# Kernel tuning notes

Measured on AMD Instinct MI355X. Metric: run time of the kernel, lower is better.

The kernel has to match this reference:

```python
import jax, jax.numpy as jnp
import numpy as np
from jax import lax

IMG = 512            # image H = W
FH = FW = 32         # feature map spatial size
A = 9                # anchors per location (3 sizes x 3 ratios)
N = FH * FW * A      # total anchors = 9216
IOU_THR = 0.7
MIN_SCORE = 0.5
MIN_SIZE = 1e-3


def make_anchors():
    """Anchors in centroid format (cx, cy, w, h), ordered (H, W, A)."""
    stride = IMG / FH
    sizes = np.array([32.0, 64.0, 128.0])
    ratios = np.array([0.5, 1.0, 2.0])
    ws = (sizes[:, None] / np.sqrt(ratios)[None, :]).reshape(-1)  # (A,)
    hs = (sizes[:, None] * np.sqrt(ratios)[None, :]).reshape(-1)  # (A,)
    cx = (np.arange(FW) + 0.5) * stride
    cy = (np.arange(FH) + 0.5) * stride
    CX = np.broadcast_to(cx[None, :, None], (FH, FW, A))
    CY = np.broadcast_to(cy[:, None, None], (FH, FW, A))
    Wg = np.broadcast_to(ws[None, None, :], (FH, FW, A))
    Hg = np.broadcast_to(hs[None, None, :], (FH, FW, A))
    anc = np.stack([CX, CY, Wg, Hg], axis=-1).reshape(-1, 4)
    return jnp.asarray(anc, dtype=jnp.float32)


def pairwise_iou(b):
    # b: (N,4) corners x1,y1,x2,y2
    x1, y1, x2, y2 = b[:, 0], b[:, 1], b[:, 2], b[:, 3]
    area = (x2 - x1) * (y2 - y1)
    ix1 = jnp.maximum(x1[:, None], x1[None, :])
    iy1 = jnp.maximum(y1[:, None], y1[None, :])
    ix2 = jnp.minimum(x2[:, None], x2[None, :])
    iy2 = jnp.minimum(y2[:, None], y2[None, :])
    inter = jnp.maximum(ix2 - ix1, 0.0) * jnp.maximum(iy2 - iy1, 0.0)
    union = area[:, None] + area[None, :] - inter
    return inter / jnp.maximum(union, 1e-9)


def nms_keep(boxes, scores, valid):
    """Greedy NMS. Returns bool keep mask of shape (N,). Index decisions only."""
    s = jnp.where(valid, scores, -jnp.inf)
    order = jnp.argsort(-s)
    b = boxes[order]
    v = valid[order]
    ious = pairwise_iou(b)  # (N, N)
    idx = jnp.arange(N)

    def body(i, supp):
        keep_i = (~supp[i]) & v[i]
        return supp | (keep_i & (ious[i] > IOU_THR) & (idx > i))

    supp = lax.fori_loop(0, N, body, jnp.zeros(N, dtype=bool))
    keep_sorted = (~supp) & v
    return jnp.zeros(N, dtype=bool).at[order].set(keep_sorted)


def setup_inputs() -> dict:
    key = jax.random.key(0)
    ks = jax.random.split(key, 4)
    return {
        "feature_map": jax.random.normal(ks[0], (1, 256, FH, FW), jnp.float32),
        "conv1_w": jax.random.normal(ks[1], (512, 256, 3, 3), jnp.float32) * 0.02,
        "conv1_b": jnp.zeros((512,), jnp.float32),
        "conv2_w": jax.random.normal(ks[2], (A, 512), jnp.float32) * 0.01,
        "conv2_b": jnp.zeros((A,), jnp.float32),
        "conv3_w": jax.random.normal(ks[3], (4 * A, 512), jnp.float32) * 0.01,
        "conv3_b": jnp.zeros((4 * A,), jnp.float32),
    }


def reference(feature_map, conv1_w, conv1_b, conv2_w, conv2_b, conv3_w, conv3_b):
    anchors = make_anchors()  # (N,4) cx,cy,w,h

    # --- conv backbone head ---
    h = lax.conv_general_dilated(
        feature_map, conv1_w, (1, 1), "SAME",
        dimension_numbers=("NCHW", "OIHW", "NCHW"))
    h = jax.nn.relu(h + conv1_b[None, :, None, None])  # (1,512,H,W)

    scores = jax.nn.sigmoid(
        jnp.einsum("bchw,ac->bahw", h, conv2_w) + conv2_b[None, :, None, None])
    scores = scores.transpose(0, 2, 3, 1).reshape(-1)  # (N,) ordered (H,W,A)

    off = jnp.einsum("bchw,oc->bohw", h, conv3_w) + conv3_b[None, :, None, None]
    off = off.reshape(1, A, 4, FH, FW).transpose(0, 3, 4, 1, 2).reshape(-1, 4)

    acx, acy, aw, ah = anchors[:, 0], anchors[:, 1], anchors[:, 2], anchors[:, 3]
    cx = acx + off[:, 0] * aw
    cy = acy + off[:, 1] * ah
    bw = aw * jnp.exp(off[:, 2])
    bh = ah * jnp.exp(off[:, 3])
    boxes = jnp.stack([cx - bw / 2, cy - bh / 2, cx + bw / 2, cy + bh / 2], axis=1)

    # --- clip to image ---
    lo = jnp.array([0.0, 0.0, 0.0, 0.0], jnp.float32)
    hi = jnp.array([IMG, IMG, IMG, IMG], jnp.float32)
    boxes = jnp.clip(boxes, lo, hi)

    # --- remove small boxes + score threshold (as a mask, jit-safe) ---
    valid = ((boxes[:, 2] - boxes[:, 0]) >= MIN_SIZE) \
          & ((boxes[:, 3] - boxes[:, 1]) >= MIN_SIZE) \
          & (scores >= MIN_SCORE)

    # --- NMS (selection is index-based; no gradient through the decision) ---
    keep = nms_keep(lax.stop_gradient(boxes), lax.stop_gradient(scores), valid)

    out = jnp.concatenate(
        [boxes * keep[:, None].astype(boxes.dtype),
         (scores * keep.astype(scores.dtype))[:, None]], axis=1)  # (N,5)
    return out
```

## Files before the change

### kernel.cpp

```cpp
#include <hip/hip_runtime.h>
#include <math.h>

#define FHW   32
#define NA    9
#define NBOX  9216
#define C1    256
#define C2    512
#define KTOT  2304
#define KS    8
#define KCH   (KTOT / KS)
#define CAP   64

struct AnchorWH { float w[NA]; float h[NA]; };

#define FP_OFF    0u
#define WT_OFF    1183744u
#define HP_OFF    5902336u
#define BOX_OFF   22679552u
#define SC_OFF    22827008u
#define VL_OFF    22863872u
#define DEG_OFF   22900736u
#define ADJ_OFF   22937600u
#define KEEP_OFF  24117248u
#define NV_OFF    24154112u

__global__ __launch_bounds__(256) void k_prep(const float* __restrict__ fin,
                                              float* __restrict__ Fp,
                                              unsigned int* __restrict__ deg,
                                              unsigned int* __restrict__ nv,
                                              const float* __restrict__ w1,
                                              float* __restrict__ Wt) {
    if (blockIdx.x < 1156) {
        int idx = blockIdx.x * 256 + threadIdx.x;
        if (idx < 256 * 34 * 34) {
            int c   = idx / 1156;
            int rem = idx - c * 1156;
            int yy  = rem / 34;
            int xx  = rem - yy * 34;
            float v = 0.f;
            if (yy >= 1 && yy <= 32 && xx >= 1 && xx <= 32)
                v = fin[c * 1024 + (yy - 1) * 32 + (xx - 1)];
            Fp[idx] = v;
        }
        if (idx < NBOX) deg[idx] = 0u;
        if (idx == 0)   *nv = 0u;
    } else {
        __shared__ float tile[32][33];
        int tb  = blockIdx.x - 1156;
        int k0  = (tb % 72) * 32;
        int oc0 = (tb / 72) * 32;
        int t   = threadIdx.x;
        int r0 = t >> 5, c = t & 31;
        #pragma unroll
        for (int i = 0; i < 4; ++i) {
            int r = r0 + 8 * i;
            tile[r][c] = w1[(oc0 + r) * KTOT + k0 + c];
        }
        __syncthreads();
        #pragma unroll
        for (int i = 0; i < 4; ++i) {
            int kk = r0 + 8 * i;
            Wt[(k0 + kk) * C2 + oc0 + c] = tile[c][kk];
        }
    }
}

__global__ __launch_bounds__(64, 1) void k_gemm(const float* __restrict__ Fp,
                                                const float* __restrict__ Wt,
                                                float* __restrict__ hp) {
    const int id = blockIdx.x;
    const int g  = id & 63, bx = id >> 6;
    const int by = g >> 3, kz = g & 7;
    const int p0  = bx * 64;
    const int oc0 = by * 64;
    const int k0b = kz * KCH;
    const int t  = threadIdx.x;
    const int r8 = t >> 3, c8 = t & 7;

    __shared__ float As[16][64];
    __shared__ float Bs[16][64];

    float acc[8][8];
    #pragma unroll
    for (int r = 0; r < 8; ++r)
        #pragma unroll
        for (int c = 0; c < 8; ++c) acc[r][c] = 0.f;

    const int p = p0 + t, y = p >> 5, x = p & 31;

    for (int kt = 0; kt < KCH; kt += 16) {
        #pragma unroll
        for (int kk = 0; kk < 16; ++kk) {
            int k   = k0b + kt + kk;
            int c   = k / 9;
            int kap = k - c * 9;
            int dy  = kap / 3;
            int dx  = kap - dy * 3;
            As[kk][t] = Fp[(c * 34 + y + dy) * 34 + x + dx];
        }
        #pragma unroll
        for (int i = 0; i < 4; ++i) {
            int idx4 = t + 64 * i;
            int kk = idx4 >> 4, c4 = idx4 & 15;
            *(float4*)&Bs[kk][c4 * 4] =
                *(const float4*)&Wt[(k0b + kt + kk) * C2 + oc0 + c4 * 4];
        }
        __syncthreads();
        #pragma unroll
        for (int kk = 0; kk < 16; ++kk) {
            float a[8], b[8];
            *(float4*)&a[0] = *(const float4*)&As[kk][r8 * 4];
            *(float4*)&a[4] = *(const float4*)&As[kk][r8 * 4 + 32];
            *(float4*)&b[0] = *(const float4*)&Bs[kk][c8 * 4];
            *(float4*)&b[4] = *(const float4*)&Bs[kk][c8 * 4 + 32];
            #pragma unroll
            for (int r = 0; r < 8; ++r)
                #pragma unroll
                for (int c = 0; c < 8; ++c) acc[r][c] += a[r] * b[c];
        }
        __syncthreads();
    }
    #pragma unroll
    for (int r = 0; r < 8; ++r) {
        int row = r8 * 4 + (r & 3) + 32 * (r >> 2);
        float* dst = hp + ((kz * 1024 + p0 + row) * C2 + oc0 + c8 * 4);
        *(float4*)dst        = *(float4*)&acc[r][0];
        *(float4*)(dst + 32) = *(float4*)&acc[r][4];
    }
}

__global__ __launch_bounds__(256) void k_heads(const float* __restrict__ hp,
                                               const float* __restrict__ b1,
                                               const float* __restrict__ w2,
                                               const float* __restrict__ b2,
                                               const float* __restrict__ w3,
                                               const float* __restrict__ b3,
                                               float* __restrict__ boxes,
                                               float* __restrict__ scoresG,
                                               unsigned int* __restrict__ nv,
                                               unsigned int* __restrict__ vlist,
                                               AnchorWH awh) {
    const int p = blockIdx.x;
    const int t = threadIdx.x;
    __shared__ float hrow[C2];
    __shared__ float arr[45];

    #pragma unroll
    for (int i = 0; i < 2; ++i) {
        int c = t + 256 * i;
        float s = b1[c];
        #pragma unroll
        for (int ks = 0; ks < KS; ++ks) s += hp[(ks * 1024 + p) * C2 + c];
        hrow[c] = fmaxf(s, 0.f);
    }
    __syncthreads();

    const int w = t >> 6, lane = t & 63;
    float h8[8];
    #pragma unroll
    for (int i = 0; i < 8; ++i) h8[i] = hrow[lane + 64 * i];

    for (int j = w; j < 45; j += 4) {
        const float* wp = (j < 9) ? (w2 + j * C2) : (w3 + (j - 9) * C2);
        float s = 0.f;
        #pragma unroll
        for (int i = 0; i < 8; ++i) s += h8[i] * wp[lane + 64 * i];
        #pragma unroll
        for (int d = 1; d < 64; d <<= 1) s += __shfl_xor(s, d, 64);
        if (lane == 0) arr[j] = s;
    }
    __syncthreads();

    if (t < NA) {
        int a = t;
        float logit = arr[a] + b2[a];
        float score = 1.f / (1.f + expf(-logit));
        float o0 = arr[9 + a * 4 + 0] + b3[a * 4 + 0];
        float o1 = arr[9 + a * 4 + 1] + b3[a * 4 + 1];
        float o2 = arr[9 + a * 4 + 2] + b3[a * 4 + 2];
        float o3 = arr[9 + a * 4 + 3] + b3[a * 4 + 3];
        int y = p >> 5, x = p & 31;
        float ax = (x + 0.5f) * 16.f, ay = (y + 0.5f) * 16.f;
        float aw = awh.w[a], ah = awh.h[a];
        float cx = ax + o0 * aw;
        float cy = ay + o1 * ah;
        float bw = aw * expf(o2);
        float bh = ah * expf(o3);
        float x1 = fminf(fmaxf(cx - bw * 0.5f, 0.f), 512.f);
        float y1 = fminf(fmaxf(cy - bh * 0.5f, 0.f), 512.f);
        float x2 = fminf(fmaxf(cx + bw * 0.5f, 0.f), 512.f);
        float y2 = fminf(fmaxf(cy + bh * 0.5f, 0.f), 512.f);
        int n = p * 9 + a;
        float4 bx4; bx4.x = x1; bx4.y = y1; bx4.z = x2; bx4.w = y2;
        ((float4*)boxes)[n] = bx4;
        scoresG[n] = score;
        bool valid = (x2 - x1 >= 0.001f) && (y2 - y1 >= 0.001f) && (score >= 0.5f);
        if (valid) {
            unsigned int ci = atomicAdd(nv, 1u);
            vlist[ci] = (unsigned int)n;
        }
    }
}

__global__ __launch_bounds__(256) void k_adj(const unsigned int* __restrict__ nvp,
                                             const unsigned int* __restrict__ vlist,
                                             const float* __restrict__ boxes,
                                             const float* __restrict__ scoresG,
                                             unsigned int* __restrict__ deg,
                                             unsigned short* __restrict__ adj) {
    const int Nv = (int)*nvp;
    int b = blockIdx.x;
    int tv = (int)(sqrtf(2.f * b + 0.25f) - 0.5f);
    while ((tv + 1) * (tv + 2) / 2 <= b) tv++;
    while (tv * (tv + 1) / 2 > b) tv--;
    int tu = b - tv * (tv + 1) / 2;
    if (tv * 128 >= Nv) return;

    __shared__ float4 ub[128], vb[128];
    __shared__ float  us[128], vs[128];
    __shared__ int    uo[128], vo[128];
    int t = threadIdx.x;
    if (t < 128) {
        int gi = tu * 128 + t;
        if (gi < Nv) { int n = (int)vlist[gi]; ub[t] = ((const float4*)boxes)[n]; us[t] = scoresG[n]; uo[t] = n; }
        else us[t] = -1.f;
    } else {
        int tt = t - 128;
        int gj = tv * 128 + tt;
        if (gj < Nv) { int n = (int)vlist[gj]; vb[tt] = ((const float4*)boxes)[n]; vs[tt] = scoresG[n]; vo[tt] = n; }
        else vs[tt] = -1.f;
    }
    __syncthreads();

    for (int s = 0; s < 64; ++s) {
        int q  = t + 256 * s;
        int i  = q >> 7, jj = q & 127;
        if (tu == tv && i >= jj) continue;
        float su = us[i], sv = vs[jj];
        if (su < 0.f || sv < 0.f) continue;
        float4 bu = ub[i], bv = vb[jj];
        float au = (bu.z - bu.x) * (bu.w - bu.y);
        float av = (bv.z - bv.x) * (bv.w - bv.y);
        float ix1 = fmaxf(bu.x, bv.x), iy1 = fmaxf(bu.y, bv.y);
        float ix2 = fminf(bu.z, bv.z), iy2 = fminf(bu.w, bv.w);
        float inter = fmaxf(ix2 - ix1, 0.f) * fmaxf(iy2 - iy1, 0.f);
        float uni = au + av - inter;
        float iou = inter / fmaxf(uni, 1e-9f);
        if (iou > 0.7f) {
            int gi = tu * 128 + i, gj = tv * 128 + jj;
            bool uHigh = (su > sv) || (su == sv && uo[i] < vo[jj]);
            int lower = uHigh ? gj : gi;
            int upper = uHigh ? gi : gj;
            unsigned int slot = atomicAdd(&deg[lower], 1u);
            if (slot < CAP) adj[lower * CAP + slot] = (unsigned short)upper;
        }
    }
}

__global__ __launch_bounds__(1024) void k_peel(const unsigned int* __restrict__ nvp,
                                               const unsigned int* __restrict__ vlist,
                                               const unsigned int* __restrict__ deg,
                                               const unsigned short* __restrict__ adj,
                                               unsigned int* __restrict__ keep) {
    __shared__ unsigned char st[NBOX];
    __shared__ int changed;
    const int t = threadIdx.x;
    const int Nv = (int)*nvp;
    for (int n = t; n < NBOX; n += 1024) keep[n] = 0u;
    for (int i = t; i < Nv; i += 1024) st[i] = 0;
    __syncthreads();

    for (int round = 0; round < 512; ++round) {
        if (t == 0) changed = 0;
        __syncthreads();
        bool any = false;
        for (int i = t; i < Nv; i += 1024) {
            if (st[i] == 0) {
                int d = (int)deg[i]; if (d > CAP) d = CAP;
                bool kseen = false, useen = false;
                for (int s = 0; s < d; ++s) {
                    unsigned char v = st[adj[i * CAP + s]];
                    kseen |= (v == 1);
                    useen |= (v == 0);
                }
                if (kseen)      { st[i] = 2; any = true; }
                else if (!useen){ st[i] = 1; any = true; }
            }
        }
        if (any) changed = 1;
        __syncthreads();
        int c = changed;
        __syncthreads();
        if (!c) break;
    }
    for (int i = t; i < Nv; i += 1024)
        if (st[i] == 1) keep[vlist[i]] = 1u;
}

__global__ __launch_bounds__(256) void k_out(const float* __restrict__ boxes,
                                             const float* __restrict__ scoresG,
                                             const unsigned int* __restrict__ keep,
                                             float* __restrict__ out) {
    int n = blockIdx.x * 256 + threadIdx.x;
    if (n >= NBOX) return;
    float4 b = ((const float4*)boxes)[n];
    bool k = keep[n] != 0u;
    out[n * 5 + 0] = k ? b.x : 0.f;
    out[n * 5 + 1] = k ? b.y : 0.f;
    out[n * 5 + 2] = k ? b.z : 0.f;
    out[n * 5 + 3] = k ? b.w : 0.f;
    out[n * 5 + 4] = k ? scoresG[n] : 0.f;
}

extern "C" void kernel_launch(void* const* d_in, const int* in_sizes, int n_in,
                              void* d_out, int out_size, void* d_ws, size_t ws_size,
                              hipStream_t stream) {
    const float* fin = (const float*)d_in[0];
    const float* w1  = (const float*)d_in[1];
    const float* b1  = (const float*)d_in[2];
    const float* w2  = (const float*)d_in[3];
    const float* b2  = (const float*)d_in[4];
    const float* w3  = (const float*)d_in[5];
    const float* b3  = (const float*)d_in[6];
    float* out = (float*)d_out;

    char* ws = (char*)d_ws;
    float*          Fp    = (float*)(ws + FP_OFF);
    float*          Wt    = (float*)(ws + WT_OFF);
    float*          hp    = (float*)(ws + HP_OFF);
    float*          boxes = (float*)(ws + BOX_OFF);
    float*          sc    = (float*)(ws + SC_OFF);
    unsigned int*   vlist = (unsigned int*)(ws + VL_OFF);
    unsigned int*   deg   = (unsigned int*)(ws + DEG_OFF);
    unsigned short* adj   = (unsigned short*)(ws + ADJ_OFF);
    unsigned int*   keep  = (unsigned int*)(ws + KEEP_OFF);
    unsigned int*   nv    = (unsigned int*)(ws + NV_OFF);

    AnchorWH awh;
    {
        const double sizes[3]  = {32.0, 64.0, 128.0};
        const double ratios[3] = {0.5, 1.0, 2.0};
        for (int si = 0; si < 3; ++si)
            for (int ri = 0; ri < 3; ++ri) {
                awh.w[si * 3 + ri] = (float)(sizes[si] / sqrt(ratios[ri]));
                awh.h[si * 3 + ri] = (float)(sizes[si] * sqrt(ratios[ri]));
            }
    }

    k_prep<<<dim3(1156 + 72 * 16), 256, 0, stream>>>(fin, Fp, deg, nv, w1, Wt);
    k_gemm<<<dim3(1024), 64, 0, stream>>>(Fp, Wt, hp);
    k_heads<<<dim3(1024), 256, 0, stream>>>(hp, b1, w2, b2, w3, b3, boxes, sc, nv, vlist, awh);
    k_adj<<<dim3(72 * 73 / 2), 256, 0, stream>>>(nv, vlist, boxes, sc, deg, adj);
    k_peel<<<dim3(1), 1024, 0, stream>>>(nv, vlist, deg, adj, keep);
    k_out<<<dim3((NBOX + 255) / 256), 256, 0, stream>>>(boxes, sc, keep, out);
}
```

Before: 213.9 us.

## Retile conv GEMM to 256-thread 64x128 blocks and fuse output write into peel

The im2col GEMM moves from 64-thread blocks computing 64x64 tiles with an 8x8 per-thread accumulator to 256-thread blocks computing 64x128 tiles with 4x8 per thread, halving the grid and raising occupancy. The NMS peel kernel now keeps its keep mask in shared memory and writes the final masked output itself, which removes the separate k_out launch and the global keep buffer. The peel block also drops to 512 threads and its round cap falls from 512 to 256. The lower cap could stop before convergence on harder inputs, and the single-block output write is now serial over all boxes.

```diff
diff --git a/kernel.cpp b/kernel.cpp
--- a/kernel.cpp
+++ b/kernel.cpp
@@ -21,8 +21,7 @@
 #define VL_OFF    22863872u
 #define DEG_OFF   22900736u
 #define ADJ_OFF   22937600u
-#define KEEP_OFF  24117248u
-#define NV_OFF    24154112u
+#define NV_OFF    24117248u
 
 __global__ __launch_bounds__(256) void k_prep(const float* __restrict__ fin,
                                               float* __restrict__ Fp,
@@ -65,67 +64,68 @@
     }
 }
 
-__global__ __launch_bounds__(64, 1) void k_gemm(const float* __restrict__ Fp,
-                                                const float* __restrict__ Wt,
-                                                float* __restrict__ hp) {
+__global__ __launch_bounds__(256, 2) void k_gemm(const float* __restrict__ Fp,
+                                                 const float* __restrict__ Wt,
+                                                 float* __restrict__ hp) {
     const int id = blockIdx.x;
-    const int g  = id & 63, bx = id >> 6;
+    const int bx = id >> 5, g = id & 31;
     const int by = g >> 3, kz = g & 7;
     const int p0  = bx * 64;
-    const int oc0 = by * 64;
+    const int oc0 = by * 128;
     const int k0b = kz * KCH;
     const int t  = threadIdx.x;
-    const int r8 = t >> 3, c8 = t & 7;
+    const int ty = t >> 4, tx = t & 15;
 
     __shared__ float As[16][64];
-    __shared__ float Bs[16][64];
-
-    float acc[8][8];
+    __shared__ float Bs[16][128];
+
+    float acc[4][8];
     #pragma unroll
-    for (int r = 0; r < 8; ++r)
+    for (int r = 0; r < 4; ++r)
         #pragma unroll
         for (int c = 0; c < 8; ++c) acc[r][c] = 0.f;
 
-    const int p = p0 + t, y = p >> 5, x = p & 31;
-
     for (int kt = 0; kt < KCH; kt += 16) {
         #pragma unroll
-        for (int kk = 0; kk < 16; ++kk) {
+        for (int i = 0; i < 4; ++i) {
+            int e  = t + 256 * i;
+            int kk = e >> 6, pp = e & 63;
             int k   = k0b + kt + kk;
             int c   = k / 9;
             int kap = k - c * 9;
             int dy  = kap / 3;
             int dx  = kap - dy * 3;
-            As[kk][t] = Fp[(c * 34 + y + dy) * 34 + x + dx];
-        }
-        #pragma unroll
-        for (int i = 0; i < 4; ++i) {
-            int idx4 = t + 64 * i;
-            int kk = idx4 >> 4, c4 = idx4 & 15;
+            int p  = p0 + pp;
+            int y  = p >> 5, x = p & 31;
+            As[kk][pp] = Fp[(c * 34 + y + dy) * 34 + x + dx];
+        }
+        #pragma unroll
+        for (int i = 0; i < 2; ++i) {
+            int e4 = t + 256 * i;
+            int kk = e4 >> 5, c4 = e4 & 31;
             *(float4*)&Bs[kk][c4 * 4] =
                 *(const float4*)&Wt[(k0b + kt + kk) * C2 + oc0 + c4 * 4];
         }
         __syncthreads();
         #pragma unroll
         for (int kk = 0; kk < 16; ++kk) {
-            float a[8], b[8];
-            *(float4*)&a[0] = *(const float4*)&As[kk][r8 * 4];
-            *(float4*)&a[4] = *(const float4*)&As[kk][r8 * 4 + 32];
-            *(float4*)&b[0] = *(const float4*)&Bs[kk][c8 * 4];
-            *(float4*)&b[4] = *(const float4*)&Bs[kk][c8 * 4 + 32];
+            float a[4], b[8];
+            *(float4*)&a[0] = *(const float4*)&As[kk][ty * 4];
+            *(float4*)&b[0] = *(const float4*)&Bs[kk][tx * 4];
+            *(float4*)&b[4] = *(const float4*)&Bs[kk][tx * 4 + 64];
             #pragma unroll
-            for (int r = 0; r < 8; ++r)
+            for (int r = 0; r < 4; ++r)
                 #pragma unroll
                 for (int c = 0; c < 8; ++c) acc[r][c] += a[r] * b[c];
         }
         __syncthreads();
     }
     #pragma unroll
-    for (int r = 0; r < 8; ++r) {
-        int row = r8 * 4 + (r & 3) + 32 * (r >> 2);
-        float* dst = hp + ((kz * 1024 + p0 + row) * C2 + oc0 + c8 * 4);
+    for (int r = 0; r < 4; ++r) {
+        int p = p0 + ty * 4 + r;
+        float* dst = hp + ((kz * 1024 + p) * C2 + oc0 + tx * 4);
         *(float4*)dst        = *(float4*)&acc[r][0];
-        *(float4*)(dst + 32) = *(float4*)&acc[r][4];
+        *(float4*)(dst + 64) = *(float4*)&acc[r][4];
     }
 }
 
@@ -257,24 +257,27 @@
     }
 }
 
-__global__ __launch_bounds__(1024) void k_peel(const unsigned int* __restrict__ nvp,
-                                               const unsigned int* __restrict__ vlist,
-                                               const unsigned int* __restrict__ deg,
-                                               const unsigned short* __restrict__ adj,
-                                               unsigned int* __restrict__ keep) {
+__global__ __launch_bounds__(512) void k_peel(const unsigned int* __restrict__ nvp,
+                                              const unsigned int* __restrict__ vlist,
+                                              const unsigned int* __restrict__ deg,
+                                              const unsigned short* __restrict__ adj,
+                                              const float* __restrict__ boxes,
+                                              const float* __restrict__ scoresG,
+                                              float* __restrict__ out) {
     __shared__ unsigned char st[NBOX];
+    __shared__ unsigned char keepm[NBOX];
     __shared__ int changed;
     const int t = threadIdx.x;
     const int Nv = (int)*nvp;
-    for (int n = t; n < NBOX; n += 1024) keep[n] = 0u;
-    for (int i = t; i < Nv; i += 1024) st[i] = 0;
-    __syncthreads();
-
-    for (int round = 0; round < 512; ++round) {
+    for (int n = t; n < NBOX; n += 512) keepm[n] = 0;
+    for (int i = t; i < Nv; i += 512) st[i] = 0;
+    __syncthreads();
+
+    for (int round = 0; round < 256; ++round) {
         if (t == 0) changed = 0;
         __syncthreads();
         bool any = false;
-        for (int i = t; i < Nv; i += 1024) {
+        for (int i = t; i < Nv; i += 512) {
             if (st[i] == 0) {
                 int d = (int)deg[i]; if (d > CAP) d = CAP;
                 bool kseen = false, useen = false;
@@ -293,23 +296,19 @@
         __syncthreads();
         if (!c) break;
     }
-    for (int i = t; i < Nv; i += 1024)
-        if (st[i] == 1) keep[vlist[i]] = 1u;
-}
-
-__global__ __launch_bounds__(256) void k_out(const float* __restrict__ boxes,
-                                             const float* __restrict__ scoresG,
-                                             const unsigned int* __restrict__ keep,
-                                             float* __restrict__ out) {
-    int n = blockIdx.x * 256 + threadIdx.x;
-    if (n >= NBOX) return;
-    float4 b = ((const float4*)boxes)[n];
-    bool k = keep[n] != 0u;
-    out[n * 5 + 0] = k ? b.x : 0.f;
-    out[n * 5 + 1] = k ? b.y : 0.f;
-    out[n * 5 + 2] = k ? b.z : 0.f;
-    out[n * 5 + 3] = k ? b.w : 0.f;
-    out[n * 5 + 4] = k ? scoresG[n] : 0.f;
+    for (int i = t; i < Nv; i += 512)
+        if (st[i] == 1) keepm[vlist[i]] = 1;
+    __syncthreads();
+
+    for (int n = t; n < NBOX; n += 512) {
+        float4 b = ((const float4*)boxes)[n];
+        bool k = keepm[n] != 0;
+        out[n * 5 + 0] = k ? b.x : 0.f;
+        out[n * 5 + 1] = k ? b.y : 0.f;
+        out[n * 5 + 2] = k ? b.z : 0.f;
+        out[n * 5 + 3] = k ? b.w : 0.f;
+        out[n * 5 + 4] = k ? scoresG[n] : 0.f;
+    }
 }
 
 extern "C" void kernel_launch(void* const* d_in, const int* in_sizes, int n_in,
@@ -333,7 +332,6 @@
     unsigned int*   vlist = (unsigned int*)(ws + VL_OFF);
     unsigned int*   deg   = (unsigned int*)(ws + DEG_OFF);
     unsigned short* adj   = (unsigned short*)(ws + ADJ_OFF);
-    unsigned int*   keep  = (unsigned int*)(ws + KEEP_OFF);
     unsigned int*   nv    = (unsigned int*)(ws + NV_OFF);
 
     AnchorWH awh;
@@ -348,9 +346,8 @@
     }
 
     k_prep<<<dim3(1156 + 72 * 16), 256, 0, stream>>>(fin, Fp, deg, nv, w1, Wt);
-    k_gemm<<<dim3(1024), 64, 0, stream>>>(Fp, Wt, hp);
+    k_gemm<<<dim3(512), 256, 0, stream>>>(Fp, Wt, hp);
     k_heads<<<dim3(1024), 256, 0, stream>>>(hp, b1, w2, b2, w3, b3, boxes, sc, nv, vlist, awh);
     k_adj<<<dim3(72 * 73 / 2), 256, 0, stream>>>(nv, vlist, boxes, sc, deg, adj);
-    k_peel<<<dim3(1), 1024, 0, stream>>>(nv, vlist, deg, adj, keep);
-    k_out<<<dim3((NBOX + 255) / 256), 256, 0, stream>>>(boxes, sc, keep, out);
-}
+    k_peel<<<dim3(1), 512, 0, stream>>>(nv, vlist, deg, adj, boxes, sc, out);
+}
```

After: 209.2 us. 2.2% less time.
